# Performance work log

Measured on AMD Instinct MI355X. Metric: run time of the kernel, lower is better.

The kernel has to match this reference:

```python
import jax, jax.numpy as jnp
import numpy as np

NUM_WORDS = 10000
IN_DIM = 300
SIZE = 256
NUM_SEQ = 2
B = 16
L = 128
NUM_BASE_LEMMAS = 3000


def _lstm(x, Wi, Wh, b):
    # x: [L, B, D] -> hidden states [L, B, H]
    Bb = x.shape[1]
    H = Wh.shape[0]
    def step(carry, xt):
        h, c = carry
        z = xt @ Wi + h @ Wh + b  # [B, 4H], gate order i,f,g,o (torch convention)
        i, f, g, o = jnp.split(z, 4, axis=-1)
        c = jax.nn.sigmoid(f) * c + jax.nn.sigmoid(i) * jnp.tanh(g)
        h = jax.nn.sigmoid(o) * jnp.tanh(c)
        return (h, c), h
    init = (jnp.zeros((Bb, H), x.dtype), jnp.zeros((Bb, H), x.dtype))
    _, hs = jax.lax.scan(step, init, x)
    return hs


def _bilstm(x, lengths, Wi_f, Wh_f, b_f, Wi_b, Wh_b, b_b):
    # x: [B, L, D]; variable-length bidirectional LSTM, concat outputs [B, L, 2H]
    Bb, Ll, _ = x.shape
    t = jnp.arange(Ll)
    # reverse the valid prefix of each row; padding stays in place
    rev_idx = jnp.where(t[None, :] < lengths[:, None], lengths[:, None] - 1 - t[None, :], t[None, :])
    x_rev = jnp.take_along_axis(x, rev_idx[:, :, None], axis=1)
    hf = _lstm(jnp.swapaxes(x, 0, 1), Wi_f, Wh_f, b_f)
    hb = _lstm(jnp.swapaxes(x_rev, 0, 1), Wi_b, Wh_b, b_b)
    hf = jnp.swapaxes(hf, 0, 1)
    hb = jnp.take_along_axis(jnp.swapaxes(hb, 0, 1), rev_idx[:, :, None], axis=1)
    return jnp.concatenate([hf, hb], axis=-1)


def setup_inputs() -> dict:
    key = jax.random.key(0)
    ks = jax.random.split(key, 16)
    d = {}
    d['word_embeddings'] = jax.random.normal(ks[0], (NUM_WORDS, IN_DIM), jnp.float32)
    # embedding projection Linear(IN_DIM, SIZE)
    d['Wp'] = jax.random.normal(ks[1], (IN_DIM, SIZE), jnp.float32) * 0.05
    d['bp'] = jnp.zeros((SIZE,), jnp.float32)
    D = SIZE + NUM_SEQ
    d['Wi_f'] = jax.random.normal(ks[2], (D, 4 * SIZE), jnp.float32) * 0.05
    d['Wh_f'] = jax.random.normal(ks[3], (SIZE, 4 * SIZE), jnp.float32) * 0.05
    d['b_f'] = jnp.zeros((4 * SIZE,), jnp.float32)
    d['Wi_b'] = jax.random.normal(ks[4], (D, 4 * SIZE), jnp.float32) * 0.05
    d['Wh_b'] = jax.random.normal(ks[5], (SIZE, 4 * SIZE), jnp.float32) * 0.05
    d['b_b'] = jnp.zeros((4 * SIZE,), jnp.float32)
    # encoded projection Linear(2*SIZE, SIZE)
    d['Wenc'] = jax.random.normal(ks[6], (2 * SIZE, SIZE), jnp.float32) * 0.05
    d['benc'] = jnp.zeros((SIZE,), jnp.float32)
    # gate projection Linear(2*SIZE, SIZE), bias init 1.0 per source
    d['Wgate'] = jax.random.normal(ks[7], (2 * SIZE, SIZE), jnp.float32) * 0.05
    d['bgate'] = jnp.ones((SIZE,), jnp.float32)
    d['seq0'] = jax.random.randint(ks[8], (B, L), 0, NUM_WORDS, jnp.int32)
    d['seq1'] = jax.random.randint(ks[9], (B, L), 0, NUM_WORDS, jnp.int32)
    d['len0'] = jax.random.randint(ks[10], (B,), 1, L + 1, jnp.int32)
    d['len1'] = jax.random.randint(ks[11], (B,), 1, L + 1, jnp.int32)
    d['u2l'] = jax.random.randint(ks[12], (NUM_WORDS,), 0, NUM_BASE_LEMMAS, jnp.int32)
    return d


def reference(word_embeddings, Wp, bp, Wi_f, Wh_f, b_f, Wi_b, Wh_b, b_b, Wenc, benc, Wgate, bgate, seq0, seq1, len0, len1, u2l):
    num_words = word_embeddings.shape[0]
    batch = seq0.shape[0]
    size = Wp.shape[1]
    we = jax.nn.relu(word_embeddings @ Wp + bp)  # [num_words, size]
    offsets = jnp.arange(batch, dtype=jnp.int32) * num_words  # [B]
    u2l_off = (u2l[None, :] + offsets[:, None]).reshape(-1)  # [B*num_words]
    num_lemmas = batch * num_words
    ctxt = jnp.tile(we, (batch, 1))  # [B*num_words, size]
    for i, (seq, lengths) in enumerate(((seq0, len0), (seq1, len1))):
        Ll = seq.shape[1]
        seq_off = seq + offsets[:, None]  # [B, L]
        enc_in = ctxt[seq_off]  # gather: [B, L, size]
        mode = jnp.zeros((batch, Ll, NUM_SEQ), enc_in.dtype).at[:, :, i].set(1.0)
        enc_in = jnp.concatenate([enc_in, mode], axis=-1)  # [B, L, size+num_seq]
        h = _bilstm(enc_in, lengths, Wi_f, Wh_f, b_f, Wi_b, Wh_b, b_b)  # [B, L, 2*size]
        enc = h @ Wenc + benc  # [B, L, size]
        mask = (jnp.arange(Ll)[None, :] < lengths[:, None]).astype(enc.dtype)
        enc = enc * mask[:, :, None]
        seq_lemmas = u2l_off[seq_off.reshape(-1)]  # [B*L]
        new_lemma = jax.ops.segment_max(enc.reshape(-1, size), seq_lemmas, num_segments=num_lemmas)
        new_lemma = jax.nn.relu(new_lemma)  # empty segments (-inf) -> 0
        new_word = new_lemma[u2l_off]  # scatter-back via gather: [B*num_words, size]
        gate = jax.nn.sigmoid(jnp.concatenate([ctxt, new_word], axis=-1) @ Wgate + bgate)
        ctxt = ctxt * gate + (1.0 - gate) * new_word
    return ctxt
```

## Files before the change

kernel.cpp:

```cpp
#include <hip/hip_runtime.h>

#define NW    10000
#define INDIM 300
#define SZ    256
#define BB    16
#define LL    128
#define NLEM  3000
#define FH    1024
#define NCAP  8192

typedef short  bf16x8 __attribute__((ext_vector_type(8)));
typedef float  f32x4  __attribute__((ext_vector_type(4)));

__device__ __forceinline__ float sigf(float x){
  return __builtin_amdgcn_rcpf(1.f+__builtin_amdgcn_exp2f(-1.442695041f*x));
}
__device__ __forceinline__ float tanhf_(float x){
  return fmaf(-2.f, __builtin_amdgcn_rcpf(1.f+__builtin_amdgcn_exp2f(2.885390082f*x)), 1.f);
}
__device__ __forceinline__ short f2b(float f){
  unsigned u=__float_as_uint(f); u += 0x7FFFu + ((u>>16)&1u); return (short)(u>>16);
}
__device__ __forceinline__ int pack2(float a, float b){
  return ((int)(unsigned short)f2b(a)) | (((int)(unsigned short)f2b(b))<<16);
}
#define B2F(s) __uint_as_float(((unsigned)(unsigned short)(s))<<16)
#define MFA(a,b,c) __builtin_amdgcn_mfma_f32_16x16x32_bf16(a,b,c,0,0,0)

__global__ void k_we(const float* __restrict__ emb, const float* __restrict__ Wp,
                     const float* __restrict__ bp, float* __restrict__ we){
  __shared__ __align__(16) float As[16][INDIM];
  int r0 = blockIdx.x*16, tid = threadIdx.x;
  for(int i=tid;i<16*INDIM;i+=256){int lr=i/INDIM,d=i-lr*INDIM;
    As[lr][d]=emb[(long)(r0+lr)*INDIM+d];}
  __syncthreads();
  int cl=tid&63, rg=tid>>6;
  float acc[4][4];
  #pragma unroll
  for(int i=0;i<4;i++){acc[i][0]=acc[i][1]=acc[i][2]=acc[i][3]=0.f;}
  for(int k=0;k<INDIM;k+=4){
    float4 a4[4];
    #pragma unroll
    for(int i=0;i<4;i++) a4[i]=*(const float4*)&As[rg*4+i][k];
    #pragma unroll
    for(int j=0;j<4;j++){
      const float* wr=Wp+(long)(k+j)*SZ+cl;
      float w0=wr[0],w1=wr[64],w2=wr[128],w3=wr[192];
      #pragma unroll
      for(int i=0;i<4;i++){
        float a=(j==0)?a4[i].x:(j==1)?a4[i].y:(j==2)?a4[i].z:a4[i].w;
        acc[i][0]=fmaf(a,w0,acc[i][0]);acc[i][1]=fmaf(a,w1,acc[i][1]);
        acc[i][2]=fmaf(a,w2,acc[i][2]);acc[i][3]=fmaf(a,w3,acc[i][3]);
      }
    }
  }
  #pragma unroll
  for(int i=0;i<4;i++){
    int r=r0+rg*4+i;
    #pragma unroll
    for(int cc=0;cc<4;cc++){int col=cl+cc*64;
      we[(long)r*SZ+col]=fmaxf(acc[i][cc]+bp[col],0.f);}
  }
}

__global__ void k_prep(const float* __restrict__ Wh_f, const float* __restrict__ Wh_b,
                       short* __restrict__ frag){
  int tid = blockIdx.x*256 + threadIdx.x;
  int l=tid&63, f=(tid>>6)&63, w=(tid>>12)&7, dir=tid>>15;
  const float* Wh = dir? Wh_b : Wh_f;
  int ks=f&7, T2=f>>3, s2=T2>>2, g=T2&3;
  int col = g*256 + w*32 + s2*16 + (l&15);
  int k0  = ks*32 + (l>>4)*8;
  short v[8];
  #pragma unroll
  for(int j=0;j<8;j++) v[j]=f2b(Wh[(long)(k0+j)*FH + col]);
  *(bf16x8*)(frag + (long)tid*8) = *(bf16x8*)v;
}

__global__ void k_prepwi(const float* __restrict__ Wi_f, const float* __restrict__ Wi_b,
                         short* __restrict__ wf){
  int tid = blockIdx.x*256 + threadIdx.x;
  int l=tid&63, ks=(tid>>6)&7, ct=(tid>>9)&63, dir=tid>>15;
  const float* Wi = dir? Wi_b : Wi_f;
  int col = ct*16 + (l&15);
  int k0  = ks*32 + (l>>4)*8;
  short v[8];
  #pragma unroll
  for(int j=0;j<8;j++) v[j]=f2b(Wi[(long)(k0+j)*FH + col]);
  *(bf16x8*)(wf + (long)tid*8) = *(bf16x8*)v;
}

__global__ void k_prepenc(const float* __restrict__ Wenc, short* __restrict__ wef){
  int tid = blockIdx.x*256 + threadIdx.x;
  int l=tid&63, ks=(tid>>6)&15, ct=tid>>10;
  int col = ct*16 + (l&15);
  int k0  = ks*32 + (l>>4)*8;
  short v[8];
  #pragma unroll
  for(int j=0;j<8;j++) v[j]=f2b(Wenc[(long)(k0+j)*SZ + col]);
  *(bf16x8*)(wef + (long)tid*8) = *(bf16x8*)v;
}

__global__ void k_xwi_mfma(const int* __restrict__ seq, const int* __restrict__ len,
                      const float* __restrict__ srcw, long bstride,
                      const float* __restrict__ ctxtT, const int* __restrict__ idxmap,
                      const float* __restrict__ Wi_f, const float* __restrict__ bvf,
                      const float* __restrict__ Wi_b, const float* __restrict__ bvb,
                      const short* __restrict__ wf, int iseq, short* __restrict__ xwo){
  __shared__ __align__(16) short As[64*264];
  __shared__ const float* rowp[64];
  int bx=blockIdx.x, dir=bx>>5, blk=bx&31, tid=threadIdx.x;
  int w=tid>>6, l=tid&63;
  if(tid<64){
    int t = blk*4 + (tid>>4), b = tid&15;
    int lb=len[b];
    int tt=(dir==0)? t : ((t<lb)? (lb-1-t) : t);
    int tok=seq[b*LL+tt];
    const float* rp;
    if(idxmap){
      int im=idxmap[b*NW+tok];
      rp = (im>=0)? ctxtT+(long)im*SZ : srcw+(long)tok*SZ;
    }else{
      rp = srcw + (long)b*bstride + (long)tok*SZ;
    }
    rowp[tid]=rp;
  }
  __syncthreads();
  for(int i2=tid;i2<64*64;i2+=256){
    int lr=i2>>6, c4=(i2&63)*4;
    float4 v=*(const float4*)(rowp[lr]+c4);
    int2 pk; pk.x=pack2(v.x,v.y); pk.y=pack2(v.z,v.w);
    *(int2*)&As[lr*264+c4]=pk;
  }
  __syncthreads();
  const float* __restrict__ Wi = dir? Wi_b : Wi_f;
  const float* __restrict__ bv = dir? bvb : bvf;
  const short* wfd = wf + (long)dir*262144;
  for(int n2=0;n2<16;n2++){
    int ct = w*16 + n2;
    const short* bfp = wfd + ((long)ct*8)*512 + l*8;
    f32x4 Z={0.f,0.f,0.f,0.f};
    f32x4 C0=Z,C1=Z,C2=Z,C3=Z;
    #pragma unroll
    for(int ks=0;ks<8;ks++){
      bf16x8 bb=*(const bf16x8*)(bfp + ks*512);
      int ao = ks*32 + (l>>4)*8;
      bf16x8 a0=*(const bf16x8*)(&As[((l&15)    )*264 + ao]);
      bf16x8 a1=*(const bf16x8*)(&As[((l&15)+16 )*264 + ao]);
      bf16x8 a2=*(const bf16x8*)(&As[((l&15)+32 )*264 + ao]);
      bf16x8 a3=*(const bf16x8*)(&As[((l&15)+48 )*264 + ao]);
      C0=MFA(a0,bb,C0); C1=MFA(a1,bb,C1); C2=MFA(a2,bb,C2); C3=MFA(a3,bb,C3);
    }
    int g=ct>>4, w2=(ct&15)>>1, s2=ct&1;
    int col = g*256 + w2*32 + s2*16 + (l&15);
    float be = Wi[(long)(SZ+iseq)*FH+col] + bv[col];
    #pragma unroll
    for(int m=0;m<4;m++){
      f32x4 Cm = (m==0)?C0:(m==1)?C1:(m==2)?C2:C3;
      long base=((((long)dir*128 + blk*4 + m)*8 + w2)*64 + (l>>4)*16 + (l&15))*32
                + s2*16 + g*4;
      int2 pk; pk.x=pack2(Cm[0]+be,Cm[1]+be); pk.y=pack2(Cm[2]+be,Cm[3]+be);
      *(int2*)(xwo+base)=pk;
    }
  }
}

__device__ __forceinline__ void rowgemm64(const float* __restrict__ A,
                                          const float* __restrict__ W,
                                          float* __restrict__ C,
                                          int n, int r0, int tid, float* Asf){
  for(int i=tid;i<64*SZ;i+=512){
    int lr=i>>8; int r=r0+lr;
    Asf[i]= (r<n)? A[(long)r*SZ+(i&255)] : 0.f;
  }
  __syncthreads();
  int cl=tid&63, rg=tid>>6;
  float acc[8][4];
  #pragma unroll
  for(int i=0;i<8;i++){acc[i][0]=acc[i][1]=acc[i][2]=acc[i][3]=0.f;}
  for(int k=0;k<SZ;k+=4){
    float4 a4[8];
    #pragma unroll
    for(int i=0;i<8;i++) a4[i]=*(const float4*)&Asf[(rg*8+i)*SZ+k];
    #pragma unroll
    for(int j=0;j<4;j++){
      const float* wr=W+(long)(k+j)*SZ+cl;
      float w0=wr[0],w1=wr[64],w2=wr[128],w3=wr[192];
      #pragma unroll
      for(int i=0;i<8;i++){
        float a=(j==0)?a4[i].x:(j==1)?a4[i].y:(j==2)?a4[i].z:a4[i].w;
        acc[i][0]=fmaf(a,w0,acc[i][0]);acc[i][1]=fmaf(a,w1,acc[i][1]);
        acc[i][2]=fmaf(a,w2,acc[i][2]);acc[i][3]=fmaf(a,w3,acc[i][3]);
      }
    }
  }
  #pragma unroll
  for(int i=0;i<8;i++){
    int r=r0+rg*8+i;
    if(r<n){
      #pragma unroll
      for(int cc=0;cc<4;cc++) C[(long)r*SZ+cl+cc*64]=acc[i][cc];
    }
  }
}

#define LDFW(f)    (*(const bf16x8*)(fr + (long)(f)*512 + l*8))
#define LDLW(i2,ks) (*(const bf16x8*)(bl + ((i2)*8+(ks))*512 + l*8))
#define DECLWT(T) bf16x8 W##T##_0=LDFW((T)*8+0),W##T##_1=LDFW((T)*8+1),W##T##_2=LDFW((T)*8+2),W##T##_3=LDFW((T)*8+3),W##T##_4=LDFW((T)*8+4),W##T##_5=LDFW((T)*8+5),W##T##_6=LDFW((T)*8+6),W##T##_7=LDFW((T)*8+7);
#define MMRT(T,Cv) { Cv=MFA(A0,W##T##_0,Cv); Cv=MFA(A1,W##T##_1,Cv); Cv=MFA(A2,W##T##_2,Cv); Cv=MFA(A3,W##T##_3,Cv); Cv=MFA(A4,W##T##_4,Cv); Cv=MFA(A5,W##T##_5,Cv); Cv=MFA(A6,W##T##_6,Cv); Cv=MFA(A7,W##T##_7,Cv); }
#define MMLT(i2,Cv) { Cv=MFA(A0,LDLW(i2,0),Cv); Cv=MFA(A1,LDLW(i2,1),Cv); Cv=MFA(A2,LDLW(i2,2),Cv); Cv=MFA(A3,LDLW(i2,3),Cv); Cv=MFA(A4,LDLW(i2,4),Cv); Cv=MFA(A5,LDLW(i2,5),Cv); Cv=MFA(A6,LDLW(i2,6),Cv); Cv=MFA(A7,LDLW(i2,7),Cv); }
#define MMST(Cv) { Cv=MFA(A0,S0,Cv); Cv=MFA(A1,S1,Cv); Cv=MFA(A2,S2,Cv); Cv=MFA(A3,S3,Cv); Cv=MFA(A4,S4,Cv); Cv=MFA(A5,S5,Cv); Cv=MFA(A6,S6,Cv); Cv=MFA(A7,S7,Cv); }
#define LOADST(f0) S0=LDFW((f0)+0); S1=LDFW((f0)+1); S2=LDFW((f0)+2); S3=LDFW((f0)+3); S4=LDFW((f0)+4); S5=LDFW((f0)+5); S6=LDFW((f0)+6); S7=LDFW((f0)+7);
#define G1(s,r,CA,CB,CC,CD,XA,XB) { \
  float zi=CA[r]+B2F(XA[r]), zf=CB[r]+B2F(XA[4+(r)]), zg=CC[r]+B2F(XB[r]), zo=CD[r]+B2F(XB[4+(r)]); \
  cst_##s##_##r = sigf(zf)*cst_##s##_##r + sigf(zi)*tanhf_(zg); \
  float hv = sigf(zo)*tanhf_(cst_##s##_##r); \
  int b_=4*(l>>4)+(r); int u_=w*32+(s)*16+(l&15); \
  hbn[b_*264+u_]=f2b(hv); }
#define GP(s,CA,CB,CC,CD,XA,XB) \
  G1(s,0,CA,CB,CC,CD,XA,XB) G1(s,1,CA,CB,CC,CD,XA,XB) \
  G1(s,2,CA,CB,CC,CD,XA,XB) G1(s,3,CA,CB,CC,CD,XA,XB)

extern __shared__ char smem_raw[];

__global__ __launch_bounds__(512,2) void k_lstm_f(
    const short* __restrict__ frag, const short* __restrict__ xq,
    short* __restrict__ hgs,
    const float* __restrict__ gA1, const float* __restrict__ gW1,
    float* __restrict__ gC1, int n1,
    const float* __restrict__ gA2, const float* __restrict__ gW2,
    float* __restrict__ gC2, const int* __restrict__ cnt2, int ncap2){
  const int bid=blockIdx.x, tid=threadIdx.x;
  if(bid>=2){
    float* Asf=(float*)smem_raw;
    int nb1=(n1+63)>>6;
    int gb=bid-2;
    if(gb<nb1){ rowgemm64(gA1,gW1,gC1,n1,gb*64,tid,Asf); }
    else if(cnt2){
      int n2=*cnt2; if(n2>ncap2)n2=ncap2;
      int r0=(gb-nb1)*64;
      if(r0<n2) rowgemm64(gA2,gW2,gC2,n2,r0,tid,Asf);
    }
    return;
  }
  const int dir=bid, w=tid>>6, l=tid&63;
  short* hb=(short*)smem_raw;
  short* bl=(short*)(smem_raw+16896)+w*8192;
  const short* fr = frag + (long)(dir*8+w)*32768;
  for(int i=tid;i<4224;i+=512) ((int*)smem_raw)[i]=0;
  #pragma unroll
  for(int c2=0;c2<16;c2++)
    *(f32x4*)(bl+c2*512+l*8) = *(const f32x4*)(fr+(long)(32+c2)*512+l*8);
  DECLWT(0) DECLWT(1) DECLWT(2) DECLWT(3)
  float cst_0_0=0,cst_0_1=0,cst_0_2=0,cst_0_3=0,
        cst_1_0=0,cst_1_1=0,cst_1_2=0,cst_1_3=0;
  __syncthreads();
  const short* xwb = xq + ((long)dir*128*8 + w)*2048 + (long)l*32;
  short* hgb = hgs + (long)dir*524288;
  const int db=tid>>5, du=(tid&31)*8;
  bf16x8 S0,S1,S2,S3,S4,S5,S6,S7;
  for(int t=0;t<LL;t++){
    const int cur=t&1, nxt=cur^1;
    LOADST(48)
    const short* xp = xwb + (long)t*16384;
    bf16x8 X0=*(const bf16x8*)(xp+0), X1=*(const bf16x8*)(xp+8);
    const short* hr = hb + cur*4224 + (l&15)*264 + (l>>4)*8;
    bf16x8 A0=*(const bf16x8*)(hr+0),   A1=*(const bf16x8*)(hr+32),
           A2=*(const bf16x8*)(hr+64),  A3=*(const bf16x8*)(hr+96),
           A4=*(const bf16x8*)(hr+128), A5=*(const bf16x8*)(hr+160),
           A6=*(const bf16x8*)(hr+192), A7=*(const bf16x8*)(hr+224);
    f32x4 Z={0.f,0.f,0.f,0.f};
    f32x4 C00=Z,C01=Z,C02=Z,C03=Z,C10=Z,C11=Z,C12=Z,C13=Z;
    MMRT(0,C00) MMRT(1,C01) MMRT(2,C02) MMRT(3,C03)
    MMLT(0,C10) MMLT(1,C11)
    MMST(C12)
    LOADST(56)
    bf16x8 X2=*(const bf16x8*)(xp+16), X3=*(const bf16x8*)(xp+24);
    short* hbn = hb + nxt*4224;
    GP(0, C00,C01,C02,C03, X0,X1)
    MMST(C13)
    GP(1, C10,C11,C12,C13, X2,X3)
    __syncthreads();
    f32x4 hv4 = *(const f32x4*)(hbn + db*264 + du);
    *(f32x4*)(hgb + ((long)t*16 + db)*256 + du) = hv4;
  }
}

__global__ void k_enc_mfma(const int* __restrict__ seq, const int* __restrict__ len,
                      const int* __restrict__ u2l, const short* __restrict__ hgs,
                      const short* __restrict__ wef, const float* __restrict__ benc,
                      unsigned int* __restrict__ lembuf, unsigned int* __restrict__ flags){
  __shared__ __align__(16) short As[64*520];
  __shared__ const short* pf16[64]; __shared__ const short* pb16[64];
  __shared__ int lem_s[64], val_s[64], b_s[64];
  int r0=blockIdx.x*64, tid=threadIdx.x, w=tid>>6, l=tid&63;
  if(tid<64){
    int r=r0+tid, b=r>>7, t=r&127, lb=len[b];
    int v=(t<lb); val_s[tid]=v; b_s[tid]=b;
    int lem=u2l[seq[r]]; lem_s[tid]=lem;
    pf16[tid]=hgs+((long)t*BB+b)*SZ;
    int tr=v? (lb-1-t) : t;
    pb16[tid]=hgs+((long)(LL+tr)*BB+b)*SZ;
    if(v) flags[(long)b*NLEM+lem]=1u;
  }
  __syncthreads();
  for(int i2=tid;i2<64*128;i2+=256){
    int lr=i2>>7, cc=(i2&127)*4;
    const short* sp=(cc<256)? pf16[lr]+cc : pb16[lr]+(cc-256);
    *(int2*)&As[lr*520+cc]=*(const int2*)sp;
  }
  __syncthreads();
  for(int n2=0;n2<4;n2++){
    int ct=w*4+n2;
    f32x4 Z={0.f,0.f,0.f,0.f};
    f32x4 C0=Z,C1=Z,C2=Z,C3=Z;
    #pragma unroll
    for(int ks=0;ks<16;ks++){
      bf16x8 bb=*(const bf16x8*)(wef+((long)(ct*16+ks))*512+l*8);
      int ao=ks*32+(l>>4)*8;
      bf16x8 a0=*(const bf16x8*)(&As[((l&15)    )*520+ao]);
      bf16x8 a1=*(const bf16x8*)(&As[((l&15)+16 )*520+ao]);
      bf16x8 a2=*(const bf16x8*)(&As[((l&15)+32 )*520+ao]);
      bf16x8 a3=*(const bf16x8*)(&As[((l&15)+48 )*520+ao]);
      C0=MFA(a0,bb,C0); C1=MFA(a1,bb,C1); C2=MFA(a2,bb,C2); C3=MFA(a3,bb,C3);
    }
    int col=ct*16+(l&15);
    float be=benc[col];
    #pragma unroll
    for(int m=0;m<4;m++){
      f32x4 Cm=(m==0)?C0:(m==1)?C1:(m==2)?C2:C3;
      #pragma unroll
      for(int reg=0;reg<4;reg++){
        int row=m*16+(l>>4)*4+reg;
        if(val_s[row]){
          float e=fmaxf(Cm[reg]+be,0.f);
          atomicMax(&lembuf[((long)b_s[row]*NLEM+lem_s[row])*SZ+col], __float_as_uint(e));
        }
      }
    }
  }
}

__global__ void k_rowgemm(const float* __restrict__ A, const float* __restrict__ W,
                          float* __restrict__ C, const unsigned int* __restrict__ flags){
  __shared__ __align__(16) float As[16][SZ];
  __shared__ int any_s;
  int r0=blockIdx.x*16, tid=threadIdx.x;
  if(tid==0){
    int a = flags? 0 : 1;
    if(flags){ for(int i=0;i<16;i++) a |= (int)flags[r0+i]; }
    any_s=a;
  }
  __syncthreads();
  if(!any_s) return;
  for(int i=tid;i<16*SZ;i+=256){int lr=i>>8,j=i&(SZ-1);As[lr][j]=A[(long)(r0+lr)*SZ+j];}
  __syncthreads();
  int cl=tid&63, rg=tid>>6;
  float acc[4][4];
  #pragma unroll
  for(int i=0;i<4;i++){acc[i][0]=acc[i][1]=acc[i][2]=acc[i][3]=0.f;}
  for(int k=0;k<SZ;k+=4){
    float4 a4[4];
    #pragma unroll
    for(int i=0;i<4;i++) a4[i]=*(const float4*)&As[rg*4+i][k];
    #pragma unroll
    for(int j=0;j<4;j++){
      const float* wr=W+(long)(k+j)*SZ+cl;
      float w0=wr[0],w1=wr[64],w2=wr[128],w3=wr[192];
      #pragma unroll
      for(int i=0;i<4;i++){
        float a=(j==0)?a4[i].x:(j==1)?a4[i].y:(j==2)?a4[i].z:a4[i].w;
        acc[i][0]=fmaf(a,w0,acc[i][0]);acc[i][1]=fmaf(a,w1,acc[i][1]);
        acc[i][2]=fmaf(a,w2,acc[i][2]);acc[i][3]=fmaf(a,w3,acc[i][3]);
      }
    }
  }
  #pragma unroll
  for(int i=0;i<4;i++){
    int r=r0+rg*4+i;
    #pragma unroll
    for(int cc=0;cc<4;cc++) C[(long)r*SZ+cl+cc*64]=acc[i][cc];
  }
}

__global__ void k_compact(const int* __restrict__ u2l, const unsigned int* __restrict__ flags,
                          int* __restrict__ cnt, int* __restrict__ list,
                          int* __restrict__ idxmap, int ncap){
  int r = blockIdx.x*256+threadIdx.x;
  if(r>=BB*NW) return;
  int b=r/NW, w=r-b*NW;
  int im=-1;
  if(flags[(long)b*NLEM+u2l[w]]){
    int idx=atomicAdd(cnt,1);
    if(idx<ncap){ list[idx]=r; im=idx; }
  }
  idxmap[r]=im;
}

__global__ void k_gate0c(const float* __restrict__ we, const float* __restrict__ P0,
                         const float* __restrict__ Q, const float* __restrict__ lembuf,
                         const int* __restrict__ u2l, const float* __restrict__ bg,
                         const int* __restrict__ cnt, const int* __restrict__ list,
                         float* __restrict__ ctxtT, int ncap){
  int n=*cnt; if(n>ncap)n=ncap;
  long idx=(long)blockIdx.x*256+threadIdx.x;
  long i=idx>>6; int k4=(int)(idx&63);
  if(i>=n) return;
  int r=list[i]; int b=r/NW, w=r-b*NW;
  int lem=u2l[w];
  long qb=((long)b*NLEM+lem)*SZ;
  float4 p =((const float4*)(P0+(long)w*SZ))[k4];
  float4 wv=((const float4*)(we+(long)w*SZ))[k4];
  float4 bgv=((const float4*)bg)[k4];
  float4 q =((const float4*)(Q+qb))[k4];
  float4 nw=((const float4*)(lembuf+qb))[k4];
  float4 o;
  { float g=sigf(p.x+q.x+bgv.x); o.x=wv.x*g+(1.f-g)*nw.x; }
  { float g=sigf(p.y+q.y+bgv.y); o.y=wv.y*g+(1.f-g)*nw.y; }
  { float g=sigf(p.z+q.z+bgv.z); o.z=wv.z*g+(1.f-g)*nw.z; }
  { float g=sigf(p.w+q.w+bgv.w); o.w=wv.w*g+(1.f-g)*nw.w; }
  ((float4*)ctxtT)[i*64+k4]=o;
}

__global__ void k_base0ip(float* __restrict__ we, const float* __restrict__ P0,
                          const float* __restrict__ bg){
  long idx=(long)blockIdx.x*256+threadIdx.x;
  if(idx>=(long)NW*SZ/4) return;
  int k4=(int)(idx&63);
  float4 wv=((float4*)we)[idx];
  float4 p =((const float4*)P0)[idx];
  float4 bgv=((const float4*)bg)[k4];
  wv.x*=sigf(p.x+bgv.x); wv.y*=sigf(p.y+bgv.y);
  wv.z*=sigf(p.z+bgv.z); wv.w*=sigf(p.w+bgv.w);
  ((float4*)we)[idx]=wv;
}

__global__ void k_gate0(const float* __restrict__ we, const float* __restrict__ P0,
                        const float* __restrict__ Q, const float* __restrict__ lembuf,
                        const int* __restrict__ u2l, const unsigned int* __restrict__ flags,
                        const float* __restrict__ bg, float* __restrict__ out){
  long idx=(long)blockIdx.x*256+threadIdx.x;
  const long TOTAL4=(long)BB*NW*SZ/4;
  if(idx>=TOTAL4) return;
  long row=idx>>6; int k4=(int)(idx&63);
  int r32=(int)row;
  int b=r32/NW, w=r32-b*NW;
  int lem=u2l[w];
  long qb=((long)b*NLEM+lem)*SZ;
  unsigned int fl=flags[(long)b*NLEM+lem];
  float4 p =((const float4*)(P0+(long)w*SZ))[k4];
  float4 wv=((const float4*)(we+(long)w*SZ))[k4];
  float4 bgv=((const float4*)bg)[k4];
  float4 q, nw;
  if(fl){ q=((const float4*)(Q+qb))[k4]; nw=((const float4*)(lembuf+qb))[k4]; }
  else  { q=make_float4(0.f,0.f,0.f,0.f); nw=q; }
  float4 o;
  { float g=sigf(p.x+q.x+bgv.x); o.x=wv.x*g+(1.f-g)*nw.x; }
  { float g=sigf(p.y+q.y+bgv.y); o.y=wv.y*g+(1.f-g)*nw.y; }
  { float g=sigf(p.z+q.z+bgv.z); o.z=wv.z*g+(1.f-g)*nw.z; }
  { float g=sigf(p.w+q.w+bgv.w); o.w=wv.w*g+(1.f-g)*nw.w; }
  ((float4*)out)[idx]=o;
}

__global__ void k_gate1e(const float* __restrict__ base0, const float* __restrict__ ctxtT,
                         const float* __restrict__ P1b, const float* __restrict__ Pt,
                         const int* __restrict__ idxmap,
                         const float* __restrict__ Q, const float* __restrict__ lembuf,
                         const int* __restrict__ u2l, const unsigned int* __restrict__ flags,
                         const float* __restrict__ bg, float* __restrict__ out){
  long idx=(long)blockIdx.x*256+threadIdx.x;
  const long TOTAL4=(long)BB*NW*SZ/4;
  if(idx>=TOTAL4) return;
  long row=idx>>6; int k4=(int)(idx&63);
  int r32=(int)row;
  int b=r32/NW, w=r32-b*NW;
  int im=idxmap[r32];
  int lem=u2l[w];
  long qb=((long)b*NLEM+lem)*SZ;
  unsigned int fl=flags[(long)b*NLEM+lem];
  float4 p, cv;
  if(im>=0){ p=((const float4*)(Pt+(long)im*SZ))[k4]; cv=((const float4*)(ctxtT+(long)im*SZ))[k4]; }
  else     { p=((const float4*)(P1b+(long)w*SZ))[k4]; cv=((const float4*)(base0+(long)w*SZ))[k4]; }
  float4 bgv=((const float4*)bg)[k4];
  float4 q, nw;
  if(fl){ q=((const float4*)(Q+qb))[k4]; nw=((const float4*)(lembuf+qb))[k4]; }
  else  { q=make_float4(0.f,0.f,0.f,0.f); nw=q; }
  float4 o;
  { float g=sigf(p.x+q.x+bgv.x); o.x=cv.x*g+(1.f-g)*nw.x; }
  { float g=sigf(p.y+q.y+bgv.y); o.y=cv.y*g+(1.f-g)*nw.y; }
  { float g=sigf(p.z+q.z+bgv.z); o.z=cv.z*g+(1.f-g)*nw.z; }
  { float g=sigf(p.w+q.w+bgv.w); o.w=cv.w*g+(1.f-g)*nw.w; }
  ((float4*)out)[idx]=o;
}

__global__ void k_gate1(const float* __restrict__ ctxt, const float* __restrict__ Wg,
                        const float* __restrict__ Q, const float* __restrict__ lembuf,
                        const int* __restrict__ u2l, const unsigned int* __restrict__ flags,
                        const float* __restrict__ bg, float* __restrict__ out){
  __shared__ __align__(16) float As[64][SZ];
  __shared__ __align__(16) float Ws[64][SZ];
  __shared__ int lem_s[64];
  int r0=blockIdx.x*64, tid=threadIdx.x;
  for(int i=tid;i<64*SZ;i+=256){int lr=i>>8,j=i&(SZ-1);
    As[lr][j]=ctxt[(long)(r0+lr)*SZ+j];}
  if(tid<64){int r=r0+tid; lem_s[tid]=u2l[r%NW];}
  int cl=tid&63, rg=tid>>6;
  float acc[16][4];
  #pragma unroll
  for(int i=0;i<16;i++){acc[i][0]=acc[i][1]=acc[i][2]=acc[i][3]=0.f;}
  for(int kb=0;kb<4;kb++){
    __syncthreads();
    for(int i=tid;i<64*SZ;i+=256){int lr=i>>8,j=i&(SZ-1);
      Ws[lr][j]=Wg[(long)(kb*64+lr)*SZ+j];}
    __syncthreads();
    for(int k=0;k<64;k+=4){
      float4 a4[16];
      #pragma unroll
      for(int i=0;i<16;i++) a4[i]=*(const float4*)&As[rg*16+i][kb*64+k];
      #pragma unroll
      for(int j=0;j<4;j++){
        float w0=Ws[k+j][cl],w1=Ws[k+j][cl+64],w2=Ws[k+j][cl+128],w3=Ws[k+j][cl+192];
        #pragma unroll
        for(int i=0;i<16;i++){
          float a=(j==0)?a4[i].x:(j==1)?a4[i].y:(j==2)?a4[i].z:a4[i].w;
          acc[i][0]=fmaf(a,w0,acc[i][0]);acc[i][1]=fmaf(a,w1,acc[i][1]);
          acc[i][2]=fmaf(a,w2,acc[i][2]);acc[i][3]=fmaf(a,w3,acc[i][3]);
        }
      }
    }
  }
  #pragma unroll
  for(int i=0;i<16;i++){
    int lr=rg*16+i, r=r0+lr, b=r/NW;
    long base=((long)b*NLEM+lem_s[lr])*SZ;
    unsigned int fl=flags[(long)b*NLEM+lem_s[lr]];
    #pragma unroll
    for(int cc=0;cc<4;cc++){
      int col=cl+cc*64;
      float qv=0.f, nw=0.f;
      if(fl){ qv=Q[base+col]; nw=lembuf[base+col]; }
      float g=sigf(acc[i][cc]+qv+bg[col]);
      out[(long)r*SZ+col]=As[lr][col]*g+(1.f-g)*nw;
    }
  }
}

extern "C" void kernel_launch(void* const* d_in, const int* in_sizes, int n_in,
                              void* d_out, int out_size, void* d_ws, size_t ws_size,
                              hipStream_t stream){
  const float* emb  =(const float*)d_in[0];
  const float* Wp   =(const float*)d_in[1];
  const float* bp   =(const float*)d_in[2];
  const float* Wi_f =(const float*)d_in[3];
  const float* Wh_f =(const float*)d_in[4];
  const float* b_f  =(const float*)d_in[5];
  const float* Wi_b =(const float*)d_in[6];
  const float* Wh_b =(const float*)d_in[7];
  const float* b_b  =(const float*)d_in[8];
  const float* Wenc =(const float*)d_in[9];
  const float* benc =(const float*)d_in[10];
  const float* Wg   =(const float*)d_in[11];
  const float* bg   =(const float*)d_in[12];
  const int*   seq0 =(const int*)d_in[13];
  const int*   seq1 =(const int*)d_in[14];
  const int*   len0 =(const int*)d_in[15];
  const int*   len1 =(const int*)d_in[16];
  const int*   u2l  =(const int*)d_in[17];

  float* ws    = (float*)d_ws;
  float* we    = ws;
  float* xwi   = we    + 2560000;
  float* ctxtT = xwi   + 2097152;
  float* hglob = xwi   + 4194304;
  float* lembuf= hglob + 1048576;
  float* flags = lembuf+ 12288000;
  float* Q     = flags + 48000;
  float* P0    = Q     + 12288000;
  short* whb   = (short*)(P0 + 2560000);
  short* wifrag= whb + 524288;
  short* wefrag= wifrag + 524288;
  int*   idxmap= (int*)(P0 + 2560000 + 262144 + 262144 + 65536);
  int*   list  = idxmap + 160000;
  int*   cnt   = list + NCAP;
  float* Ptouch= (float*)(cnt + 4);
  long base_floats = (long)(Ptouch - ws);
  long avail = ((long)(ws_size/4) - base_floats)/SZ;
  int sparse_ok = (avail >= NCAP);
  float* out   = (float*)d_out;

  hipFuncSetAttribute((const void*)k_lstm_f,
                      hipFuncAttributeMaxDynamicSharedMemorySize, 147968);

  k_we<<<NW/16,256,0,stream>>>(emb,Wp,bp,we);
  k_prep<<<256,256,0,stream>>>(Wh_f,Wh_b,whb);
  k_prepwi<<<256,256,0,stream>>>(Wi_f,Wi_b,wifrag);
  k_prepenc<<<64,256,0,stream>>>(Wenc,wefrag);

  const int NB1=(NW+63)/64;

  hipMemsetAsync(lembuf,0,(size_t)(12288000+48000)*4,stream);
  k_xwi_mfma<<<64,256,0,stream>>>(seq0,len0,we,0L,nullptr,nullptr,
                                  Wi_f,b_f,Wi_b,b_b,wifrag,0,(short*)xwi);
  k_lstm_f<<<2+NB1,512,147968,stream>>>(whb,(const short*)xwi,(short*)hglob,
                                        we,Wg,P0,NW,
                                        nullptr,nullptr,nullptr,nullptr,0);
  k_enc_mfma<<<BB*LL/64,256,0,stream>>>(seq0,len0,u2l,(const short*)hglob,wefrag,benc,
                                        (unsigned int*)lembuf,(unsigned int*)flags);
  k_rowgemm<<<BB*NLEM/16,256,0,stream>>>(lembuf,Wg+(long)SZ*SZ,Q,
                                         (const unsigned int*)flags);
  if(sparse_ok){
    hipMemsetAsync(cnt,0,4,stream);
    k_compact<<<(BB*NW+255)/256,256,0,stream>>>(u2l,(const unsigned int*)flags,
                                                cnt,list,idxmap,NCAP);
    k_gate0c<<<NCAP*64/256,256,0,stream>>>(we,P0,Q,lembuf,u2l,bg,cnt,list,ctxtT,NCAP);
    k_base0ip<<<(NW*SZ/4+255)/256,256,0,stream>>>(we,P0,bg);
  }else{
    long nb=((long)BB*NW*SZ/4+255)/256;
    k_gate0<<<(int)nb,256,0,stream>>>(we,P0,Q,lembuf,u2l,
                                      (const unsigned int*)flags,bg,out);
  }

  hipMemsetAsync(lembuf,0,(size_t)(12288000+48000)*4,stream);
  if(sparse_ok){
    k_xwi_mfma<<<64,256,0,stream>>>(seq1,len1,we,0L,ctxtT,idxmap,
                                    Wi_f,b_f,Wi_b,b_b,wifrag,1,(short*)xwi);
    k_lstm_f<<<2+NB1+NCAP/64,512,147968,stream>>>(whb,(const short*)xwi,(short*)hglob,
                                                  we,Wg,P0,NW,
                                                  ctxtT,Wg,Ptouch,cnt,NCAP);
  }else{
    k_xwi_mfma<<<64,256,0,stream>>>(seq1,len1,out,(long)NW*SZ,nullptr,nullptr,
                                    Wi_f,b_f,Wi_b,b_b,wifrag,1,(short*)xwi);
    k_lstm_f<<<2,512,147968,stream>>>(whb,(const short*)xwi,(short*)hglob,
                                      nullptr,nullptr,nullptr,0,
                                      nullptr,nullptr,nullptr,nullptr,0);
  }
  k_enc_mfma<<<BB*LL/64,256,0,stream>>>(seq1,len1,u2l,(const short*)hglob,wefrag,benc,
                                        (unsigned int*)lembuf,(unsigned int*)flags);
  k_rowgemm<<<BB*NLEM/16,256,0,stream>>>(lembuf,Wg+(long)SZ*SZ,Q,
                                         (const unsigned int*)flags);
  if(sparse_ok){
    long nb=((long)BB*NW*SZ/4+255)/256;
    k_gate1e<<<(int)nb,256,0,stream>>>(we,ctxtT,P0,Ptouch,idxmap,Q,lembuf,u2l,
                                       (const unsigned int*)flags,bg,out);
  }else{
    k_gate1<<<BB*NW/64,256,0,stream>>>(out,Wg,Q,lembuf,u2l,
                                       (const unsigned int*)flags,bg,out);
  }
}
```

Baseline: 1.264 ms.

## Replace lemma-buffer memsets with sparse zeroing folded into LSTM kernel blocks

Drops the two full memsets of the large lemma buffer and the count memset. Extra blocks are appended to the LSTM launch: they zero only the lemma rows touched by the sequences, plus the flags and the count, so this work overlaps the serial LSTM recurrence. The four weight-prep kernels are merged into one launch, and the fp32 embedding projection is replaced by a bf16 MFMA kernel. The costs are lower precision on the embedding projection and a reliance on untouched lemma rows never being read.

```diff
diff --git a/kernel.cpp b/kernel.cpp
--- a/kernel.cpp
+++ b/kernel.cpp
@@ -8,6 +8,7 @@
 #define NLEM  3000
 #define FH    1024
 #define NCAP  8192
+#define NB1   157
 
 typedef short  bf16x8 __attribute__((ext_vector_type(8)));
 typedef float  f32x4  __attribute__((ext_vector_type(4)));
@@ -27,78 +28,97 @@
 #define B2F(s) __uint_as_float(((unsigned)(unsigned short)(s))<<16)
 #define MFA(a,b,c) __builtin_amdgcn_mfma_f32_16x16x32_bf16(a,b,c,0,0,0)
 
-__global__ void k_we(const float* __restrict__ emb, const float* __restrict__ Wp,
-                     const float* __restrict__ bp, float* __restrict__ we){
-  __shared__ __align__(16) float As[16][INDIM];
-  int r0 = blockIdx.x*16, tid = threadIdx.x;
-  for(int i=tid;i<16*INDIM;i+=256){int lr=i/INDIM,d=i-lr*INDIM;
-    As[lr][d]=emb[(long)(r0+lr)*INDIM+d];}
-  __syncthreads();
-  int cl=tid&63, rg=tid>>6;
-  float acc[4][4];
-  #pragma unroll
-  for(int i=0;i<4;i++){acc[i][0]=acc[i][1]=acc[i][2]=acc[i][3]=0.f;}
-  for(int k=0;k<INDIM;k+=4){
-    float4 a4[4];
-    #pragma unroll
-    for(int i=0;i<4;i++) a4[i]=*(const float4*)&As[rg*4+i][k];
-    #pragma unroll
-    for(int j=0;j<4;j++){
-      const float* wr=Wp+(long)(k+j)*SZ+cl;
-      float w0=wr[0],w1=wr[64],w2=wr[128],w3=wr[192];
+__global__ void k_prepall(const float* __restrict__ Wh_f, const float* __restrict__ Wh_b,
+                          short* __restrict__ whb,
+                          const float* __restrict__ Wi_f, const float* __restrict__ Wi_b,
+                          short* __restrict__ wif,
+                          const float* __restrict__ Wenc, short* __restrict__ wef,
+                          const float* __restrict__ Wp, short* __restrict__ wpf){
+  int bx=blockIdx.x, thr=threadIdx.x;
+  if(bx<256){
+    int tid=bx*256+thr;
+    int l=tid&63, f=(tid>>6)&63, w=(tid>>12)&7, dir=tid>>15;
+    const float* Wh = dir? Wh_b : Wh_f;
+    int ks=f&7, T2=f>>3, s2=T2>>2, g=T2&3;
+    int col = g*256 + w*32 + s2*16 + (l&15);
+    int k0  = ks*32 + (l>>4)*8;
+    short v[8];
+    #pragma unroll
+    for(int j=0;j<8;j++) v[j]=f2b(Wh[(long)(k0+j)*FH + col]);
+    *(bf16x8*)(whb + (long)tid*8) = *(bf16x8*)v;
+  }else if(bx<512){
+    int tid=(bx-256)*256+thr;
+    int l=tid&63, ks=(tid>>6)&7, ct=(tid>>9)&63, dir=tid>>15;
+    const float* Wi = dir? Wi_b : Wi_f;
+    int col = ct*16 + (l&15);
+    int k0  = ks*32 + (l>>4)*8;
+    short v[8];
+    #pragma unroll
+    for(int j=0;j<8;j++) v[j]=f2b(Wi[(long)(k0+j)*FH + col]);
+    *(bf16x8*)(wif + (long)tid*8) = *(bf16x8*)v;
+  }else if(bx<576){
+    int tid=(bx-512)*256+thr;
+    int l=tid&63, ks=(tid>>6)&15, ct=tid>>10;
+    int col = ct*16 + (l&15);
+    int k0  = ks*32 + (l>>4)*8;
+    short v[8];
+    #pragma unroll
+    for(int j=0;j<8;j++) v[j]=f2b(Wenc[(long)(k0+j)*SZ + col]);
+    *(bf16x8*)(wef + (long)tid*8) = *(bf16x8*)v;
+  }else{
+    int tid2=(bx-576)*256+thr;
+    int l=tid2&63, frow=tid2>>6;
+    int ct=frow/10, ks=frow-ct*10;
+    int col=ct*16+(l&15);
+    int k0=ks*32+(l>>4)*8;
+    short v[8];
+    #pragma unroll
+    for(int j=0;j<8;j++){ int k=k0+j; v[j]=(k<INDIM)? f2b(Wp[(long)k*SZ+col]) : (short)0; }
+    *(bf16x8*)(wpf + (long)frow*512 + l*8) = *(bf16x8*)v;
+  }
+}
+
+__global__ void k_we_mfma(const float* __restrict__ emb, const short* __restrict__ wpf,
+                          const float* __restrict__ bp, float* __restrict__ we){
+  __shared__ __align__(16) short As[64*328];
+  int r0=blockIdx.x*64, tid=threadIdx.x, w=tid>>6, l=tid&63;
+  for(int i=tid;i<64*160;i+=256){
+    int lr=i/160, c2=(i-lr*160)*2;
+    int row=r0+lr;
+    float e0=0.f,e1=0.f;
+    if(row<NW){
+      if(c2<INDIM)   e0=emb[(long)row*INDIM+c2];
+      if(c2+1<INDIM) e1=emb[(long)row*INDIM+c2+1];
+    }
+    *(int*)&As[lr*328+c2]=pack2(e0,e1);
+  }
+  __syncthreads();
+  for(int n2=0;n2<4;n2++){
+    int ct=w*4+n2;
+    f32x4 Z={0.f,0.f,0.f,0.f};
+    f32x4 C0=Z,C1=Z,C2=Z,C3=Z;
+    #pragma unroll
+    for(int ks=0;ks<10;ks++){
+      bf16x8 bb=*(const bf16x8*)(wpf+((long)(ct*10+ks))*512+l*8);
+      int ao=ks*32+(l>>4)*8;
+      bf16x8 a0=*(const bf16x8*)(&As[((l&15)    )*328+ao]);
+      bf16x8 a1=*(const bf16x8*)(&As[((l&15)+16 )*328+ao]);
+      bf16x8 a2=*(const bf16x8*)(&As[((l&15)+32 )*328+ao]);
+      bf16x8 a3=*(const bf16x8*)(&As[((l&15)+48 )*328+ao]);
+      C0=MFA(a0,bb,C0); C1=MFA(a1,bb,C1); C2=MFA(a2,bb,C2); C3=MFA(a3,bb,C3);
+    }
+    int col=ct*16+(l&15);
+    float be=bp[col];
+    #pragma unroll
+    for(int m=0;m<4;m++){
+      f32x4 Cm=(m==0)?C0:(m==1)?C1:(m==2)?C2:C3;
       #pragma unroll
-      for(int i=0;i<4;i++){
-        float a=(j==0)?a4[i].x:(j==1)?a4[i].y:(j==2)?a4[i].z:a4[i].w;
-        acc[i][0]=fmaf(a,w0,acc[i][0]);acc[i][1]=fmaf(a,w1,acc[i][1]);
-        acc[i][2]=fmaf(a,w2,acc[i][2]);acc[i][3]=fmaf(a,w3,acc[i][3]);
+      for(int reg=0;reg<4;reg++){
+        int row=r0+m*16+(l>>4)*4+reg;
+        if(row<NW) we[(long)row*SZ+col]=fmaxf(Cm[reg]+be,0.f);
       }
     }
   }
-  #pragma unroll
-  for(int i=0;i<4;i++){
-    int r=r0+rg*4+i;
-    #pragma unroll
-    for(int cc=0;cc<4;cc++){int col=cl+cc*64;
-      we[(long)r*SZ+col]=fmaxf(acc[i][cc]+bp[col],0.f);}
-  }
-}
-
-__global__ void k_prep(const float* __restrict__ Wh_f, const float* __restrict__ Wh_b,
-                       short* __restrict__ frag){
-  int tid = blockIdx.x*256 + threadIdx.x;
-  int l=tid&63, f=(tid>>6)&63, w=(tid>>12)&7, dir=tid>>15;
-  const float* Wh = dir? Wh_b : Wh_f;
-  int ks=f&7, T2=f>>3, s2=T2>>2, g=T2&3;
-  int col = g*256 + w*32 + s2*16 + (l&15);
-  int k0  = ks*32 + (l>>4)*8;
-  short v[8];
-  #pragma unroll
-  for(int j=0;j<8;j++) v[j]=f2b(Wh[(long)(k0+j)*FH + col]);
-  *(bf16x8*)(frag + (long)tid*8) = *(bf16x8*)v;
-}
-
-__global__ void k_prepwi(const float* __restrict__ Wi_f, const float* __restrict__ Wi_b,
-                         short* __restrict__ wf){
-  int tid = blockIdx.x*256 + threadIdx.x;
-  int l=tid&63, ks=(tid>>6)&7, ct=(tid>>9)&63, dir=tid>>15;
-  const float* Wi = dir? Wi_b : Wi_f;
-  int col = ct*16 + (l&15);
-  int k0  = ks*32 + (l>>4)*8;
-  short v[8];
-  #pragma unroll
-  for(int j=0;j<8;j++) v[j]=f2b(Wi[(long)(k0+j)*FH + col]);
-  *(bf16x8*)(wf + (long)tid*8) = *(bf16x8*)v;
-}
-
-__global__ void k_prepenc(const float* __restrict__ Wenc, short* __restrict__ wef){
-  int tid = blockIdx.x*256 + threadIdx.x;
-  int l=tid&63, ks=(tid>>6)&15, ct=tid>>10;
-  int col = ct*16 + (l&15);
-  int k0  = ks*32 + (l>>4)*8;
-  short v[8];
-  #pragma unroll
-  for(int j=0;j<8;j++) v[j]=f2b(Wenc[(long)(k0+j)*SZ + col]);
-  *(bf16x8*)(wef + (long)tid*8) = *(bf16x8*)v;
 }
 
 __global__ void k_xwi_mfma(const int* __restrict__ seq, const int* __restrict__ len,
@@ -229,17 +249,47 @@
     const float* __restrict__ gA1, const float* __restrict__ gW1,
     float* __restrict__ gC1, int n1,
     const float* __restrict__ gA2, const float* __restrict__ gW2,
-    float* __restrict__ gC2, const int* __restrict__ cnt2, int ncap2){
+    float* __restrict__ gC2, const int* __restrict__ cnt2, int ncap2,
+    const int* __restrict__ zsA, const int* __restrict__ zsB,
+    const int* __restrict__ u2l, float* __restrict__ lemz,
+    int* __restrict__ flagz, int* __restrict__ cntz){
   const int bid=blockIdx.x, tid=threadIdx.x;
   if(bid>=2){
+    int gb=bid-2;
     float* Asf=(float*)smem_raw;
-    int nb1=(n1+63)>>6;
-    int gb=bid-2;
-    if(gb<nb1){ rowgemm64(gA1,gW1,gC1,n1,gb*64,tid,Asf); }
-    else if(cnt2){
+    int nb1 = gA1 ? (n1+63)>>6 : 0;
+    if(gb<nb1){ rowgemm64(gA1,gW1,gC1,n1,gb*64,tid,Asf); return; }
+    gb-=nb1;
+    int nb2 = gA2 ? (ncap2>>6) : 0;
+    if(gb<nb2){
       int n2=*cnt2; if(n2>ncap2)n2=ncap2;
-      int r0=(gb-nb1)*64;
+      int r0=gb*64;
       if(r0<n2) rowgemm64(gA2,gW2,gC2,n2,r0,tid,Asf);
+      return;
+    }
+    gb-=nb2;
+    if(zsA){
+      if(gb<256){
+        int r8=gb*8+(tid>>6); int b=r8>>7, t=r8&127;
+        int lem=u2l[zsA[b*LL+t]];
+        *(float4*)(lemz+((long)b*NLEM+lem)*SZ+(tid&63)*4)=make_float4(0.f,0.f,0.f,0.f);
+        return;
+      }
+      gb-=256;
+    }
+    if(zsB){
+      if(gb<256){
+        int r8=gb*8+(tid>>6); int b=r8>>7, t=r8&127;
+        int lem=u2l[zsB[b*LL+t]];
+        *(float4*)(lemz+((long)b*NLEM+lem)*SZ+(tid&63)*4)=make_float4(0.f,0.f,0.f,0.f);
+        return;
+      }
+      gb-=256;
+    }
+    {
+      int idx=gb*512+tid;
+      if(idx<12000) ((int4*)flagz)[idx]=make_int4(0,0,0,0);
+      if(cntz && gb==0 && tid==0) *cntz=0;
     }
     return;
   }
@@ -579,7 +629,8 @@
   short* whb   = (short*)(P0 + 2560000);
   short* wifrag= whb + 524288;
   short* wefrag= wifrag + 524288;
-  int*   idxmap= (int*)(P0 + 2560000 + 262144 + 262144 + 65536);
+  short* wpfrag= wefrag + 131072;
+  int*   idxmap= (int*)(P0 + 2560000 + 262144 + 262144 + 65536 + 40960);
   int*   list  = idxmap + 160000;
   int*   cnt   = list + NCAP;
   float* Ptouch= (float*)(cnt + 4);
@@ -591,25 +642,20 @@
   hipFuncSetAttribute((const void*)k_lstm_f,
                       hipFuncAttributeMaxDynamicSharedMemorySize, 147968);
 
-  k_we<<<NW/16,256,0,stream>>>(emb,Wp,bp,we);
-  k_prep<<<256,256,0,stream>>>(Wh_f,Wh_b,whb);
-  k_prepwi<<<256,256,0,stream>>>(Wi_f,Wi_b,wifrag);
-  k_prepenc<<<64,256,0,stream>>>(Wenc,wefrag);
-
-  const int NB1=(NW+63)/64;
-
-  hipMemsetAsync(lembuf,0,(size_t)(12288000+48000)*4,stream);
+  k_prepall<<<616,256,0,stream>>>(Wh_f,Wh_b,whb, Wi_f,Wi_b,wifrag,
+                                  Wenc,wefrag, Wp,wpfrag);
+  k_we_mfma<<<NB1,256,0,stream>>>(emb,wpfrag,bp,we);
+
   k_xwi_mfma<<<64,256,0,stream>>>(seq0,len0,we,0L,nullptr,nullptr,
                                   Wi_f,b_f,Wi_b,b_b,wifrag,0,(short*)xwi);
-  k_lstm_f<<<2+NB1,512,147968,stream>>>(whb,(const short*)xwi,(short*)hglob,
-                                        we,Wg,P0,NW,
-                                        nullptr,nullptr,nullptr,nullptr,0);
+  k_lstm_f<<<2+NB1+256+24,512,147968,stream>>>(whb,(const short*)xwi,(short*)hglob,
+      we,Wg,P0,NW, nullptr,nullptr,nullptr,nullptr,0,
+      seq0,nullptr,u2l,lembuf,(int*)flags,cnt);
   k_enc_mfma<<<BB*LL/64,256,0,stream>>>(seq0,len0,u2l,(const short*)hglob,wefrag,benc,
                                         (unsigned int*)lembuf,(unsigned int*)flags);
   k_rowgemm<<<BB*NLEM/16,256,0,stream>>>(lembuf,Wg+(long)SZ*SZ,Q,
                                          (const unsigned int*)flags);
   if(sparse_ok){
-    hipMemsetAsync(cnt,0,4,stream);
     k_compact<<<(BB*NW+255)/256,256,0,stream>>>(u2l,(const unsigned int*)flags,
                                                 cnt,list,idxmap,NCAP);
     k_gate0c<<<NCAP*64/256,256,0,stream>>>(we,P0,Q,lembuf,u2l,bg,cnt,list,ctxtT,NCAP);
@@ -620,19 +666,18 @@
                                       (const unsigned int*)flags,bg,out);
   }
 
-  hipMemsetAsync(lembuf,0,(size_t)(12288000+48000)*4,stream);
   if(sparse_ok){
     k_xwi_mfma<<<64,256,0,stream>>>(seq1,len1,we,0L,ctxtT,idxmap,
                                     Wi_f,b_f,Wi_b,b_b,wifrag,1,(short*)xwi);
-    k_lstm_f<<<2+NB1+NCAP/64,512,147968,stream>>>(whb,(const short*)xwi,(short*)hglob,
-                                                  we,Wg,P0,NW,
-                                                  ctxtT,Wg,Ptouch,cnt,NCAP);
+    k_lstm_f<<<2+NB1+NCAP/64+256+256+24,512,147968,stream>>>(whb,(const short*)xwi,
+        (short*)hglob, we,Wg,P0,NW, ctxtT,Wg,Ptouch,cnt,NCAP,
+        seq0,seq1,u2l,lembuf,(int*)flags,nullptr);
   }else{
     k_xwi_mfma<<<64,256,0,stream>>>(seq1,len1,out,(long)NW*SZ,nullptr,nullptr,
                                     Wi_f,b_f,Wi_b,b_b,wifrag,1,(short*)xwi);
-    k_lstm_f<<<2,512,147968,stream>>>(whb,(const short*)xwi,(short*)hglob,
-                                      nullptr,nullptr,nullptr,0,
-                                      nullptr,nullptr,nullptr,nullptr,0);
+    k_lstm_f<<<2+256+256+24,512,147968,stream>>>(whb,(const short*)xwi,(short*)hglob,
+        nullptr,nullptr,nullptr,0, nullptr,nullptr,nullptr,nullptr,0,
+        seq0,seq1,u2l,lembuf,(int*)flags,nullptr);
   }
   k_enc_mfma<<<BB*LL/64,256,0,stream>>>(seq1,len1,u2l,(const short*)hglob,wefrag,benc,
                                         (unsigned int*)lembuf,(unsigned int*)flags);
```

Measured after the change: 1.261 ms. Within noise of the previous version (-0.3%).
